# Kernel tuning notes

Measured on AMD Instinct MI355X. Metric: run time of the kernel, lower is better.

The kernel has to match this reference:

```python
import jax, jax.numpy as jnp
import numpy as np

NS = 100000   # served nodes
NI = 100000   # interfered nodes
E = 1000000   # edges per relation
D = 64        # 2 * Nt_num, Nt_num = 32
HM = 32       # message MLP hidden
HU = 16       # update MLP hidden


def _lin_init(key, fan_in, fan_out):
    s = 1.0 / np.sqrt(fan_in)
    kw, kb = jax.random.split(key)
    w = jax.random.uniform(kw, (fan_in, fan_out), jnp.float32, -s, s)
    b = jax.random.uniform(kb, (fan_out,), jnp.float32, -s, s)
    return w, b


def setup_inputs() -> dict:
    key = jax.random.key(0)
    ks = jax.random.split(key, 12)
    wm1, bm1 = _lin_init(ks[0], D, HM)
    wm2, bm2 = _lin_init(ks[1], HM, D)
    wu1, bu1 = _lin_init(ks[2], D, HU)
    wu2, bu2 = _lin_init(ks[3], HU, D)
    wo, bo = _lin_init(ks[4], D, D)
    edge_s2i = jnp.stack([
        jax.random.randint(ks[5], (E,), 0, NS),   # src in served
        jax.random.randint(ks[6], (E,), 0, NI),   # dst in interfered
    ]).astype(jnp.int64)
    edge_i2s = jnp.stack([
        jax.random.randint(ks[7], (E,), 0, NI),   # src in interfered
        jax.random.randint(ks[8], (E,), 0, NS),   # dst in served
    ]).astype(jnp.int64)
    return {
        "x_served": jax.random.normal(ks[9], (NS, D), jnp.float32),
        "x_interfered": jax.random.normal(ks[10], (NI, D), jnp.float32),
        "edge_s2i": edge_s2i,
        "edge_i2s": edge_i2s,
        "wm1": wm1, "bm1": bm1, "wm2": wm2, "bm2": bm2,
        "wu1": wu1, "bu1": bu1, "wu2": wu2, "bu2": bu2,
        "wo": wo, "bo": bo,
    }


def reference(x_served, x_interfered, edge_s2i, edge_i2s,
              wm1, bm1, wm2, bm2, wu1, bu1, wu2, bu2, wo, bo):
    def mlp_m(h):  # MLP([D, 32, D]): Lin+ReLU, Lin+ReLU
        return jax.nn.relu(jax.nn.relu(h @ wm1 + bm1) @ wm2 + bm2)

    def mlp_u(h):  # MLP([D, 16, D])
        return jax.nn.relu(jax.nn.relu(h @ wu1 + bu1) @ wu2 + bu2)

    def conv(x_src, edges, n_dst):
        # gather source node features per edge, per-edge message MLP
        msg = mlp_m(x_src[edges[0]])                    # [E, D]
        # scatter-sum into destination nodes
        agg = jax.ops.segment_sum(msg, edges[1], num_segments=n_dst)
        return mlp_u(agg)                               # [n_dst, D]

    xs, xi = x_served, x_interfered
    for _ in range(3):
        new_i = conv(xs, edge_s2i, NI)   # served -> interfered
        new_s = conv(xi, edge_i2s, NS)   # interfered -> served
        xs, xi = new_s, new_i
    # h2o on served: Lin + Tanh -> beamforming matrix
    return jnp.tanh(xs @ wo + bo)
```

## Files before the change

kernel.cpp:

```cpp
#include <hip/hip_runtime.h>
#include <hip/hip_fp16.h>
#include <math.h>

constexpr int D = 64;
constexpr int CAP = 48;
constexpr int RPB = 256;
constexpr int EPB = 8192;

typedef _Float16 half2_t __attribute__((ext_vector_type(2)));
typedef _Float16 f16x8 __attribute__((ext_vector_type(8)));
typedef float f32x4 __attribute__((ext_vector_type(4)));

__device__ inline float fdot2(unsigned a, unsigned b, float c){
    return __builtin_amdgcn_fdot2(__builtin_bit_cast(half2_t, a),
                                  __builtin_bit_cast(half2_t, b), c, false);
}

__device__ inline unsigned pack2(float lo, float hi){
    __half2 h = __floats2half2_rn(lo, hi);
    return *(unsigned*)&h;
}

__device__ inline void ld16u(const unsigned* base, unsigned* w){
    const uint4* p = (const uint4*)base;
    uint4 a = p[0], b = p[1], c = p[2], d = p[3];
    w[0]=a.x;  w[1]=a.y;  w[2]=a.z;  w[3]=a.w;
    w[4]=b.x;  w[5]=b.y;  w[6]=b.z;  w[7]=b.w;
    w[8]=c.x;  w[9]=c.y;  w[10]=c.z; w[11]=c.w;
    w[12]=d.x; w[13]=d.y; w[14]=d.z; w[15]=d.w;
}

__device__ inline void store_half8(__half* dst, const float* o){
    uint4 w;
    w.x = pack2(o[0], o[1]); w.y = pack2(o[2], o[3]);
    w.z = pack2(o[4], o[5]); w.w = pack2(o[6], o[7]);
    *((uint4*)dst) = w;
}

__device__ inline void load_half8(const __half* src, float* r){
    uint4 w = *((const uint4*)src);
    __half2* h = (__half2*)&w;
    float2 f0 = __half22float2(h[0]);
    float2 f1 = __half22float2(h[1]);
    float2 f2 = __half22float2(h[2]);
    float2 f3 = __half22float2(h[3]);
    r[0] = f0.x; r[1] = f0.y; r[2] = f1.x; r[3] = f1.y;
    r[4] = f2.x; r[5] = f2.y; r[6] = f3.x; r[7] = f3.y;
}


__global__ void k_zero(int* __restrict__ p, int n){
    for (int i = threadIdx.x; i < n; i += 256) p[i] = 0;
}


__global__ void __launch_bounds__(512) k_bucket_mlpm(
        const int* __restrict__ es2i, const int* __restrict__ ei2s, int E, int NI,
        int NBUK, int BSTRIDE,
        int* __restrict__ gcur, unsigned* __restrict__ buckets,
        const float* __restrict__ x,
        const float* __restrict__ wm1, const float* __restrict__ bm1,
        const float* __restrict__ wm2, const float* __restrict__ bm2,
        __half* __restrict__ y, int Nmlp, int nbEdge)
{
    __shared__ __align__(16) char smem[8704];
    int t = threadIdx.x;

    if ((int)blockIdx.x < nbEdge){
        int* hist = (int*)smem;
        int* base = (int*)(smem + 4096);
        for (int i = t; i < NBUK; i += 512) hist[i] = 0;
        __syncthreads();
        int e0 = blockIdx.x * EPB + t;
        int rr[16], ss[16];
        #pragma unroll
        for (int k = 0; k < 16; k++){
            int i = e0 + k*512;
            if (i < E){
                ss[k] = es2i[i];            rr[k] = es2i[E + i];
            } else if (i < 2*E){
                int j = i - E;
                ss[k] = ei2s[j];            rr[k] = NI + ei2s[E + j];
            } else rr[k] = -1;
        }
        #pragma unroll
        for (int k = 0; k < 16; k++)
            if (rr[k] >= 0) atomicAdd(&hist[rr[k] >> 8], 1);
        __syncthreads();
        for (int b = t; b < NBUK; b += 512){
            int h = hist[b];
            base[b] = h ? atomicAdd(&gcur[b], h) : 0;
        }
        __syncthreads();
        #pragma unroll
        for (int k = 0; k < 16; k++){
            if (rr[k] >= 0){
                int b = rr[k] >> 8;
                int p = atomicAdd(&base[b], 1);
                if (p < BSTRIDE)
                    buckets[(size_t)b*BSTRIDE + p] =
                        ((unsigned)(rr[k] & 255) << 24) | (unsigned)ss[k];
            }
        }
        return;
    }

    unsigned* w1p = (unsigned*)smem;
    unsigned* w2p = (unsigned*)(smem + 4096);
    float*    sb1 = (float*)(smem + 8192);
    float*    sb2 = (float*)(smem + 8320);
    for (int i = t; i < 1024; i += 512){ int kp=i>>5, j=i&31; w1p[i]=pack2(wm1[(2*kp)*32+j], wm1[(2*kp+1)*32+j]); }
    for (int i = t; i < 1024; i += 512){ int jp=i>>6, c=i&63; w2p[i]=pack2(wm2[(2*jp)*64+c], wm2[(2*jp+1)*64+c]); }
    if (t < 32) sb1[t] = bm1[t];
    else if (t >= 64 && t < 128) sb2[t - 64] = bm2[t - 64];
    __syncthreads();
    int n = ((int)blockIdx.x - nbEdge)*512 + t;
    if (n >= Nmlp) return;

    const float4* xp = (const float4*)(x + (size_t)n*D);
    unsigned xq[32];
    #pragma unroll
    for (int i = 0; i < 16; i++){
        float4 v = xp[i];
        xq[2*i]   = pack2(v.x, v.y);
        xq[2*i+1] = pack2(v.z, v.w);
    }
    float h[32];
    #pragma unroll
    for (int j = 0; j < 32; j++) h[j] = 0.f;
    #pragma unroll
    for (int kp = 0; kp < 32; kp++){
        unsigned xv = xq[kp];
        unsigned w[32];
        ld16u(&w1p[kp*32],      w);
        ld16u(&w1p[kp*32 + 16], w + 16);
        #pragma unroll
        for (int j = 0; j < 32; j++) h[j] = fdot2(xv, w[j], h[j]);
    }
    #pragma unroll
    for (int j = 0; j < 32; j++) h[j] = fmaxf(h[j] + sb1[j], 0.f);
    unsigned hh[16];
    #pragma unroll
    for (int jp = 0; jp < 16; jp++) hh[jp] = pack2(h[2*jp], h[2*jp+1]);

    __half* yrow = y + (size_t)n*D;
    #pragma unroll
    for (int c0 = 0; c0 < 64; c0 += 32){
        float o[32];
        #pragma unroll
        for (int c = 0; c < 32; c++) o[c] = sb2[c0 + c];
        #pragma unroll
        for (int jp = 0; jp < 16; jp++){
            unsigned hv = hh[jp];
            unsigned w[32];
            ld16u(&w2p[jp*64 + c0],      w);
            ld16u(&w2p[jp*64 + c0 + 16], w + 16);
            #pragma unroll
            for (int c = 0; c < 32; c++) o[c] = fdot2(hv, w[c], o[c]);
        }
        #pragma unroll
        for (int c = 0; c < 32; c++) o[c] = fmaxf(o[c], 0.f);
        store_half8(yrow + c0,      &o[0]);
        store_half8(yrow + c0 + 8,  &o[8]);
        store_half8(yrow + c0 + 16, &o[16]);
        store_half8(yrow + c0 + 24, &o[24]);
    }
}


__global__ void __launch_bounds__(512) k_scatter_lds(const int* __restrict__ gcur,
        const unsigned* __restrict__ buckets, int BSTRIDE, int NTOT,
        int* __restrict__ cnt, int* __restrict__ slots)
{
    __shared__ int lcnt[RPB];
    __shared__ int lslots[RPB*CAP];
    int t = threadIdx.x;
    int b = blockIdx.x;
    int r0 = b * RPB;
    int nrows = NTOT - r0; if (nrows > RPB) nrows = RPB;

    for (int i = t; i < RPB; i += 512) lcnt[i] = 0;
    __syncthreads();

    int n = gcur[b]; if (n > BSTRIDE) n = BSTRIDE;
    const unsigned* bp = buckets + (size_t)b*BSTRIDE;
    for (int k = t; k < n; k += 512){
        unsigned e = bp[k];
        int lr  = e >> 24;
        int src = e & 0xFFFFFF;
        int pos = atomicAdd(&lcnt[lr], 1);
        if (pos < CAP) lslots[lr*CAP + pos] = src;
    }
    __syncthreads();

    int4* gs = (int4*)(slots + (size_t)r0*CAP);
    const int4* ls = (const int4*)lslots;
    int n4 = nrows*CAP/4;
    for (int i = t; i < n4; i += 512) gs[i] = ls[i];
    for (int i = t; i < nrows; i += 512) cnt[r0 + i] = lcnt[i];
}


__global__ void __launch_bounds__(256) k_agg(const __half* __restrict__ M,
        const int* __restrict__ cnt, const int* __restrict__ slots,
        __half* __restrict__ agg, int N)
{
    int gid  = blockIdx.x*256 + threadIdx.x;
    int node = gid >> 6;
    if (node >= N) return;
    int lane = gid & 63;
    int sub  = lane >> 3;
    int fl   = lane & 7;
    int deg = cnt[node]; deg = deg < CAP ? deg : CAP;
    const int* row = slots + (size_t)node*CAP;
    float acc[8];
    #pragma unroll
    for (int i = 0; i < 8; i++) acc[i] = 0.f;
    for (int k = sub; k < deg; k += 8){
        int s = row[k];
        float v[8];
        load_half8(M + (size_t)s*D + fl*8, v);
        #pragma unroll
        for (int i = 0; i < 8; i++) acc[i] += v[i];
    }
    #pragma unroll
    for (int i = 0; i < 8; i++){
        acc[i] += __shfl_xor(acc[i], 8);
        acc[i] += __shfl_xor(acc[i], 16);
        acc[i] += __shfl_xor(acc[i], 32);
    }
    if (sub == 0) store_half8(agg + (size_t)node*D + fl*8, acc);
}


__global__ void __launch_bounds__(256) k_mlp_um(const __half* __restrict__ agg,
        const float* __restrict__ wu1, const float* __restrict__ bu1,
        const float* __restrict__ wu2, const float* __restrict__ bu2,
        const float* __restrict__ wm1, const float* __restrict__ bm1,
        const float* __restrict__ wm2, const float* __restrict__ bm2,
        __half* __restrict__ y, int N)
{
    __shared__ float  lds_h [4][16][20];
    __shared__ float  lds_y [4][16][68];
    __shared__ float  lds_hm[4][16][36];
    __shared__ __half lds_m [4][16][72];

    int t  = threadIdx.x;
    int wv = t >> 6, l = t & 63;
    int m  = l & 15, g = l >> 4;

    f16x8 Bu1[2], Bu2[4], Bm1[2][2], Bm2[4];
    #pragma unroll
    for (int kt = 0; kt < 2; kt++)
        #pragma unroll
        for (int i = 0; i < 8; i++)
            Bu1[kt][i] = (_Float16)wu1[(kt*32 + 8*g + i)*16 + m];
    #pragma unroll
    for (int jb = 0; jb < 4; jb++)
        #pragma unroll
        for (int i = 0; i < 8; i++){
            int k = 8*g + i;
            Bu2[jb][i] = (k < 16) ? (_Float16)wu2[k*64 + jb*16 + m] : (_Float16)0.f;
        }
    #pragma unroll
    for (int kt = 0; kt < 2; kt++)
        #pragma unroll
        for (int nt = 0; nt < 2; nt++)
            #pragma unroll
            for (int i = 0; i < 8; i++)
                Bm1[kt][nt][i] = (_Float16)wm1[(kt*32 + 8*g + i)*32 + nt*16 + m];
    #pragma unroll
    for (int jb = 0; jb < 4; jb++)
        #pragma unroll
        for (int i = 0; i < 8; i++)
            Bm2[jb][i] = (_Float16)wm2[(8*g + i)*64 + jb*16 + m];

    float bu1v = bu1[m];
    float bu2v[4], bm2v[4], bm1v[2];
    #pragma unroll
    for (int jb = 0; jb < 4; jb++){ bu2v[jb] = bu2[jb*16 + m]; bm2v[jb] = bm2[jb*16 + m]; }
    #pragma unroll
    for (int nt = 0; nt < 2; nt++) bm1v[nt] = bm1[nt*16 + m];

    #pragma unroll
    for (int tile = 0; tile < 2; tile++){
        int nb = blockIdx.x*128 + tile*64 + wv*16;
        if (nb >= N) break;

        int an = nb + m; if (an >= N) an = N - 1;
        const __half* arow = agg + (size_t)an*64;
        f16x8 Ax0 = *reinterpret_cast<const f16x8*>(arow + 8*g);
        f16x8 Ax1 = *reinterpret_cast<const f16x8*>(arow + 32 + 8*g);

        f32x4 acc = {0.f, 0.f, 0.f, 0.f};
        acc = __builtin_amdgcn_mfma_f32_16x16x32_f16(Ax0, Bu1[0], acc, 0, 0, 0);
        acc = __builtin_amdgcn_mfma_f32_16x16x32_f16(Ax1, Bu1[1], acc, 0, 0, 0);
        #pragma unroll
        for (int r = 0; r < 4; r++)
            lds_h[wv][4*g + r][m] = fmaxf(acc[r] + bu1v, 0.f);

        f16x8 Ah;
        #pragma unroll
        for (int i = 0; i < 8; i++){
            int k = 8*g + i;
            Ah[i] = (k < 16) ? (_Float16)lds_h[wv][m][k] : (_Float16)0.f;
        }

        #pragma unroll
        for (int jb = 0; jb < 4; jb++){
            f32x4 a2 = {0.f, 0.f, 0.f, 0.f};
            a2 = __builtin_amdgcn_mfma_f32_16x16x32_f16(Ah, Bu2[jb], a2, 0, 0, 0);
            #pragma unroll
            for (int r = 0; r < 4; r++)
                lds_y[wv][4*g + r][jb*16 + m] = fmaxf(a2[r] + bu2v[jb], 0.f);
        }

        f16x8 Ay0, Ay1;
        #pragma unroll
        for (int i = 0; i < 8; i++){
            Ay0[i] = (_Float16)lds_y[wv][m][8*g + i];
            Ay1[i] = (_Float16)lds_y[wv][m][32 + 8*g + i];
        }

        #pragma unroll
        for (int nt = 0; nt < 2; nt++){
            f32x4 a3 = {0.f, 0.f, 0.f, 0.f};
            a3 = __builtin_amdgcn_mfma_f32_16x16x32_f16(Ay0, Bm1[0][nt], a3, 0, 0, 0);
            a3 = __builtin_amdgcn_mfma_f32_16x16x32_f16(Ay1, Bm1[1][nt], a3, 0, 0, 0);
            #pragma unroll
            for (int r = 0; r < 4; r++)
                lds_hm[wv][4*g + r][nt*16 + m] = fmaxf(a3[r] + bm1v[nt], 0.f);
        }

        f16x8 Ahm;
        #pragma unroll
        for (int i = 0; i < 8; i++)
            Ahm[i] = (_Float16)lds_hm[wv][m][8*g + i];

        #pragma unroll
        for (int jb = 0; jb < 4; jb++){
            f32x4 a4 = {0.f, 0.f, 0.f, 0.f};
            a4 = __builtin_amdgcn_mfma_f32_16x16x32_f16(Ahm, Bm2[jb], a4, 0, 0, 0);
            #pragma unroll
            for (int r = 0; r < 4; r++)
                lds_m[wv][4*g + r][jb*16 + m] = __float2half(fmaxf(a4[r] + bm2v[jb], 0.f));
        }

        int lr = l >> 2;
        int node = nb + lr;
        if (node < N){
            uint4* dst = (uint4*)(y + (size_t)node*64);
            const uint4* src = (const uint4*)&lds_m[wv][lr][0];
            int c = l & 3;
            dst[c]     = src[c];
            dst[c + 4] = src[c + 4];
        }
    }
}


__device__ inline float fast_tanh(float x){
    float ax = fabsf(x);
    float e  = __expf(2.f*ax);
    float t  = 1.f - 2.f/(e + 1.f);
    return copysignf(t, x);
}

__global__ void __launch_bounds__(256) k_mlp_uo(const __half* __restrict__ agg,
        const float* __restrict__ wu1, const float* __restrict__ bu1,
        const float* __restrict__ wu2, const float* __restrict__ bu2,
        const float* __restrict__ wo,  const float* __restrict__ bo,
        float* __restrict__ out, int N)
{
    __shared__ float lds_h[4][16][20];
    __shared__ float lds_y[4][16][68];
    __shared__ float lds_o[4][16][68];

    int t  = threadIdx.x;
    int wv = t >> 6, l = t & 63;
    int m  = l & 15, g = l >> 4;

    f16x8 Bu1[2], Bu2[4], Bo[2][4];
    #pragma unroll
    for (int kt = 0; kt < 2; kt++)
        #pragma unroll
        for (int i = 0; i < 8; i++)
            Bu1[kt][i] = (_Float16)wu1[(kt*32 + 8*g + i)*16 + m];
    #pragma unroll
    for (int jb = 0; jb < 4; jb++)
        #pragma unroll
        for (int i = 0; i < 8; i++){
            int k = 8*g + i;
            Bu2[jb][i] = (k < 16) ? (_Float16)wu2[k*64 + jb*16 + m] : (_Float16)0.f;
        }
    #pragma unroll
    for (int kt = 0; kt < 2; kt++)
        #pragma unroll
        for (int jb = 0; jb < 4; jb++)
            #pragma unroll
            for (int i = 0; i < 8; i++)
                Bo[kt][jb][i] = (_Float16)wo[(kt*32 + 8*g + i)*64 + jb*16 + m];

    float bu1v = bu1[m];
    float bu2v[4], bov[4];
    #pragma unroll
    for (int jb = 0; jb < 4; jb++){ bu2v[jb] = bu2[jb*16 + m]; bov[jb] = bo[jb*16 + m]; }

    #pragma unroll
    for (int tile = 0; tile < 2; tile++){
        int nb = blockIdx.x*128 + tile*64 + wv*16;
        if (nb >= N) break;

        int an = nb + m; if (an >= N) an = N - 1;
        const __half* arow = agg + (size_t)an*64;
        f16x8 Ax0 = *reinterpret_cast<const f16x8*>(arow + 8*g);
        f16x8 Ax1 = *reinterpret_cast<const f16x8*>(arow + 32 + 8*g);

        f32x4 acc = {0.f, 0.f, 0.f, 0.f};
        acc = __builtin_amdgcn_mfma_f32_16x16x32_f16(Ax0, Bu1[0], acc, 0, 0, 0);
        acc = __builtin_amdgcn_mfma_f32_16x16x32_f16(Ax1, Bu1[1], acc, 0, 0, 0);
        #pragma unroll
        for (int r = 0; r < 4; r++)
            lds_h[wv][4*g + r][m] = fmaxf(acc[r] + bu1v, 0.f);

        f16x8 Ah;
        #pragma unroll
        for (int i = 0; i < 8; i++){
            int k = 8*g + i;
            Ah[i] = (k < 16) ? (_Float16)lds_h[wv][m][k] : (_Float16)0.f;
        }

        #pragma unroll
        for (int jb = 0; jb < 4; jb++){
            f32x4 a2 = {0.f, 0.f, 0.f, 0.f};
            a2 = __builtin_amdgcn_mfma_f32_16x16x32_f16(Ah, Bu2[jb], a2, 0, 0, 0);
            #pragma unroll
            for (int r = 0; r < 4; r++)
                lds_y[wv][4*g + r][jb*16 + m] = fmaxf(a2[r] + bu2v[jb], 0.f);
        }

        f16x8 Ay0, Ay1;
        #pragma unroll
        for (int i = 0; i < 8; i++){
            Ay0[i] = (_Float16)lds_y[wv][m][8*g + i];
            Ay1[i] = (_Float16)lds_y[wv][m][32 + 8*g + i];
        }

        #pragma unroll
        for (int jb = 0; jb < 4; jb++){
            f32x4 a3 = {0.f, 0.f, 0.f, 0.f};
            a3 = __builtin_amdgcn_mfma_f32_16x16x32_f16(Ay0, Bo[0][jb], a3, 0, 0, 0);
            a3 = __builtin_amdgcn_mfma_f32_16x16x32_f16(Ay1, Bo[1][jb], a3, 0, 0, 0);
            #pragma unroll
            for (int r = 0; r < 4; r++)
                lds_o[wv][4*g + r][jb*16 + m] = fast_tanh(a3[r] + bov[jb]);
        }

        int lr = l >> 2;
        int node = nb + lr;
        if (node < N){
            float4* dst = (float4*)(out + (size_t)node*64);
            const float4* src = (const float4*)&lds_o[wv][lr][0];
            int c = l & 3;
            dst[c]      = src[c];
            dst[c + 4]  = src[c + 4];
            dst[c + 8]  = src[c + 8];
            dst[c + 12] = src[c + 12];
        }
    }
}


extern "C" void kernel_launch(void* const* d_in, const int* in_sizes, int n_in,
                              void* d_out, int out_size, void* d_ws, size_t ws_size,
                              hipStream_t stream)
{
    const float* x_interfered = (const float*)d_in[1];
    const int*   e_s2i        = (const int*)d_in[2];
    const int*   e_i2s        = (const int*)d_in[3];
    const float* wm1 = (const float*)d_in[4];  const float* bm1 = (const float*)d_in[5];
    const float* wm2 = (const float*)d_in[6];  const float* bm2 = (const float*)d_in[7];
    const float* wu1 = (const float*)d_in[8];  const float* bu1 = (const float*)d_in[9];
    const float* wu2 = (const float*)d_in[10]; const float* bu2 = (const float*)d_in[11];
    const float* wo  = (const float*)d_in[12]; const float* bo  = (const float*)d_in[13];

    const int NS = in_sizes[0] / D;
    const int NI = in_sizes[1] / D;
    const int E  = in_sizes[2] / 2;
    const int NMAX = (NS > NI) ? NS : NI;
    const int NTOT = NI + NS;

    const int NBUK = ((NTOT - 1) >> 8) + 1;
    int avg = (2*E) / NBUK;
    const int BSTRIDE = ((2*avg) + 1023) & ~1023;

    char* p = (char*)d_ws;
    auto alloc = [&](size_t bytes) -> void* {
        void* r = (void*)p;
        p += (bytes + 255) & ~(size_t)255;
        return r;
    };
    __half*   M      = (__half*)alloc((size_t)NMAX*D*2);
    __half*   AGG    = (__half*)alloc((size_t)NMAX*D*2);
    int*      cnt    = (int*)alloc((size_t)NTOT*4);
    int*      gcur   = (int*)alloc((size_t)NBUK*4);
    int*      slots  = (int*)alloc((size_t)NTOT*CAP*4);
    unsigned* buckets= (unsigned*)alloc((size_t)NBUK*BSTRIDE*4);
    (void)ws_size; (void)n_in; (void)out_size;

    const int* cnt_i = cnt;
    const int* cnt_s = cnt + NI;
    const int* slots_i = slots;
    const int* slots_s = slots + (size_t)NI*CAP;

    k_zero<<<1, 256, 0, stream>>>(gcur, NBUK);

    const int nbEdge = (2*E + EPB - 1)/EPB;
    const int nbMlp  = (NI + 511)/512;
    k_bucket_mlpm<<<nbEdge + nbMlp, 512, 0, stream>>>(
        e_s2i, e_i2s, E, NI, NBUK, BSTRIDE, gcur, buckets,
        x_interfered, wm1, bm1, wm2, bm2, M, NI, nbEdge);
    k_scatter_lds<<<NBUK, 512, 0, stream>>>(gcur, buckets, BSTRIDE, NTOT, cnt, slots);

    k_agg<<<((size_t)NS*64 + 255)/256, 256, 0, stream>>>(M, cnt_s, slots_s, AGG, NS);
    k_mlp_um<<<(NS + 127)/128, 256, 0, stream>>>(AGG, wu1, bu1, wu2, bu2,
                                               wm1, bm1, wm2, bm2, M, NS);
    k_agg<<<((size_t)NI*64 + 255)/256, 256, 0, stream>>>(M, cnt_i, slots_i, AGG, NI);
    k_mlp_um<<<(NI + 127)/128, 256, 0, stream>>>(AGG, wu1, bu1, wu2, bu2,
                                               wm1, bm1, wm2, bm2, M, NI);
    k_agg<<<((size_t)NS*64 + 255)/256, 256, 0, stream>>>(M, cnt_s, slots_s, AGG, NS);
    k_mlp_uo<<<(NS + 127)/128, 256, 0, stream>>>(AGG, wu1, bu1, wu2, bu2,
                                               wo, bo, (float*)d_out, NS);
}
```

Before: 219.7 us.

## Fuse neighbor aggregation into update/message MLP kernels with ping-pong buffers

Removes the separate aggregation kernel and performs the gather-sum of neighbor messages inside the MLP kernel, writing the aggregate to LDS instead of global memory. Each lane group now sums a 16-feature slice serially over all neighbors of one node, and double buffers replace the in-place M/AGG pair. This drops an intermediate global round-trip and three launches. In exchange, aggregation parallelism per node falls: 4 lanes per node walk the degree loop sequentially instead of 64 lanes splitting edges, which lengthens the gather latency chain.

```diff
diff --git a/kernel.cpp b/kernel.cpp
--- a/kernel.cpp
+++ b/kernel.cpp
@@ -10,11 +10,6 @@
 typedef _Float16 half2_t __attribute__((ext_vector_type(2)));
 typedef _Float16 f16x8 __attribute__((ext_vector_type(8)));
 typedef float f32x4 __attribute__((ext_vector_type(4)));
-
-__device__ inline float fdot2(unsigned a, unsigned b, float c){
-    return __builtin_amdgcn_fdot2(__builtin_bit_cast(half2_t, a),
-                                  __builtin_bit_cast(half2_t, b), c, false);
-}
 
 __device__ inline unsigned pack2(float lo, float hi){
     __half2 h = __floats2half2_rn(lo, hi);
@@ -28,6 +23,11 @@
     w[4]=b.x;  w[5]=b.y;  w[6]=b.z;  w[7]=b.w;
     w[8]=c.x;  w[9]=c.y;  w[10]=c.z; w[11]=c.w;
     w[12]=d.x; w[13]=d.y; w[14]=d.z; w[15]=d.w;
+}
+
+__device__ inline float fdot2(unsigned a, unsigned b, float c){
+    return __builtin_amdgcn_fdot2(__builtin_bit_cast(half2_t, a),
+                                  __builtin_bit_cast(half2_t, b), c, false);
 }
 
 __device__ inline void store_half8(__half* dst, const float* o){
@@ -201,45 +201,15 @@
 }
 
 
-__global__ void __launch_bounds__(256) k_agg(const __half* __restrict__ M,
+__global__ void __launch_bounds__(256) k_conv_um(const __half* __restrict__ Msrc,
         const int* __restrict__ cnt, const int* __restrict__ slots,
-        __half* __restrict__ agg, int N)
-{
-    int gid  = blockIdx.x*256 + threadIdx.x;
-    int node = gid >> 6;
-    if (node >= N) return;
-    int lane = gid & 63;
-    int sub  = lane >> 3;
-    int fl   = lane & 7;
-    int deg = cnt[node]; deg = deg < CAP ? deg : CAP;
-    const int* row = slots + (size_t)node*CAP;
-    float acc[8];
-    #pragma unroll
-    for (int i = 0; i < 8; i++) acc[i] = 0.f;
-    for (int k = sub; k < deg; k += 8){
-        int s = row[k];
-        float v[8];
-        load_half8(M + (size_t)s*D + fl*8, v);
-        #pragma unroll
-        for (int i = 0; i < 8; i++) acc[i] += v[i];
-    }
-    #pragma unroll
-    for (int i = 0; i < 8; i++){
-        acc[i] += __shfl_xor(acc[i], 8);
-        acc[i] += __shfl_xor(acc[i], 16);
-        acc[i] += __shfl_xor(acc[i], 32);
-    }
-    if (sub == 0) store_half8(agg + (size_t)node*D + fl*8, acc);
-}
-
-
-__global__ void __launch_bounds__(256) k_mlp_um(const __half* __restrict__ agg,
         const float* __restrict__ wu1, const float* __restrict__ bu1,
         const float* __restrict__ wu2, const float* __restrict__ bu2,
         const float* __restrict__ wm1, const float* __restrict__ bm1,
         const float* __restrict__ wm2, const float* __restrict__ bm2,
-        __half* __restrict__ y, int N)
+        __half* __restrict__ Mdst, int N)
 {
+    __shared__ __half lds_x [4][16][72];
     __shared__ float  lds_h [4][16][20];
     __shared__ float  lds_y [4][16][68];
     __shared__ float  lds_hm[4][16][36];
@@ -287,17 +257,35 @@
         int nb = blockIdx.x*128 + tile*64 + wv*16;
         if (nb >= N) break;
 
-        int an = nb + m; if (an >= N) an = N - 1;
-        const __half* arow = agg + (size_t)an*64;
-        f16x8 Ax0 = *reinterpret_cast<const f16x8*>(arow + 8*g);
-        f16x8 Ax1 = *reinterpret_cast<const f16x8*>(arow + 32 + 8*g);
-
-        f32x4 acc = {0.f, 0.f, 0.f, 0.f};
-        acc = __builtin_amdgcn_mfma_f32_16x16x32_f16(Ax0, Bu1[0], acc, 0, 0, 0);
-        acc = __builtin_amdgcn_mfma_f32_16x16x32_f16(Ax1, Bu1[1], acc, 0, 0, 0);
+        float acc[16];
+        #pragma unroll
+        for (int i = 0; i < 16; i++) acc[i] = 0.f;
+        int node = nb + m;
+        if (node < N){
+            int deg = cnt[node]; deg = deg < CAP ? deg : CAP;
+            const int* row = slots + (size_t)node*CAP;
+            for (int k = 0; k < deg; k++){
+                int s = row[k];
+                const __half* mr = Msrc + (size_t)s*64 + g*16;
+                float v[16];
+                load_half8(mr,     v);
+                load_half8(mr + 8, v + 8);
+                #pragma unroll
+                for (int i = 0; i < 16; i++) acc[i] += v[i];
+            }
+        }
+        store_half8(&lds_x[wv][m][g*16],     acc);
+        store_half8(&lds_x[wv][m][g*16 + 8], acc + 8);
+
+        f16x8 Ax0 = *reinterpret_cast<const f16x8*>(&lds_x[wv][m][8*g]);
+        f16x8 Ax1 = *reinterpret_cast<const f16x8*>(&lds_x[wv][m][32 + 8*g]);
+
+        f32x4 a1 = {0.f, 0.f, 0.f, 0.f};
+        a1 = __builtin_amdgcn_mfma_f32_16x16x32_f16(Ax0, Bu1[0], a1, 0, 0, 0);
+        a1 = __builtin_amdgcn_mfma_f32_16x16x32_f16(Ax1, Bu1[1], a1, 0, 0, 0);
         #pragma unroll
         for (int r = 0; r < 4; r++)
-            lds_h[wv][4*g + r][m] = fmaxf(acc[r] + bu1v, 0.f);
+            lds_h[wv][4*g + r][m] = fmaxf(a1[r] + bu1v, 0.f);
 
         f16x8 Ah;
         #pragma unroll
@@ -347,9 +335,9 @@
         }
 
         int lr = l >> 2;
-        int node = nb + lr;
-        if (node < N){
-            uint4* dst = (uint4*)(y + (size_t)node*64);
+        int wnode = nb + lr;
+        if (wnode < N){
+            uint4* dst = (uint4*)(Mdst + (size_t)wnode*64);
             const uint4* src = (const uint4*)&lds_m[wv][lr][0];
             int c = l & 3;
             dst[c]     = src[c];
@@ -366,15 +354,17 @@
     return copysignf(t, x);
 }
 
-__global__ void __launch_bounds__(256) k_mlp_uo(const __half* __restrict__ agg,
+__global__ void __launch_bounds__(256) k_conv_uo(const __half* __restrict__ Msrc,
+        const int* __restrict__ cnt, const int* __restrict__ slots,
         const float* __restrict__ wu1, const float* __restrict__ bu1,
         const float* __restrict__ wu2, const float* __restrict__ bu2,
         const float* __restrict__ wo,  const float* __restrict__ bo,
         float* __restrict__ out, int N)
 {
-    __shared__ float lds_h[4][16][20];
-    __shared__ float lds_y[4][16][68];
-    __shared__ float lds_o[4][16][68];
+    __shared__ __half lds_x[4][16][72];
+    __shared__ float  lds_h[4][16][20];
+    __shared__ float  lds_y[4][16][68];
+    __shared__ float  lds_o[4][16][68];
 
     int t  = threadIdx.x;
     int wv = t >> 6, l = t & 63;
@@ -411,17 +401,35 @@
         int nb = blockIdx.x*128 + tile*64 + wv*16;
         if (nb >= N) break;
 
-        int an = nb + m; if (an >= N) an = N - 1;
-        const __half* arow = agg + (size_t)an*64;
-        f16x8 Ax0 = *reinterpret_cast<const f16x8*>(arow + 8*g);
-        f16x8 Ax1 = *reinterpret_cast<const f16x8*>(arow + 32 + 8*g);
-
-        f32x4 acc = {0.f, 0.f, 0.f, 0.f};
-        acc = __builtin_amdgcn_mfma_f32_16x16x32_f16(Ax0, Bu1[0], acc, 0, 0, 0);
-        acc = __builtin_amdgcn_mfma_f32_16x16x32_f16(Ax1, Bu1[1], acc, 0, 0, 0);
+        float acc[16];
+        #pragma unroll
+        for (int i = 0; i < 16; i++) acc[i] = 0.f;
+        int node = nb + m;
+        if (node < N){
+            int deg = cnt[node]; deg = deg < CAP ? deg : CAP;
+            const int* row = slots + (size_t)node*CAP;
+            for (int k = 0; k < deg; k++){
+                int s = row[k];
+                const __half* mr = Msrc + (size_t)s*64 + g*16;
+                float v[16];
+                load_half8(mr,     v);
+                load_half8(mr + 8, v + 8);
+                #pragma unroll
+                for (int i = 0; i < 16; i++) acc[i] += v[i];
+            }
+        }
+        store_half8(&lds_x[wv][m][g*16],     acc);
+        store_half8(&lds_x[wv][m][g*16 + 8], acc + 8);
+
+        f16x8 Ax0 = *reinterpret_cast<const f16x8*>(&lds_x[wv][m][8*g]);
+        f16x8 Ax1 = *reinterpret_cast<const f16x8*>(&lds_x[wv][m][32 + 8*g]);
+
+        f32x4 a1 = {0.f, 0.f, 0.f, 0.f};
+        a1 = __builtin_amdgcn_mfma_f32_16x16x32_f16(Ax0, Bu1[0], a1, 0, 0, 0);
+        a1 = __builtin_amdgcn_mfma_f32_16x16x32_f16(Ax1, Bu1[1], a1, 0, 0, 0);
         #pragma unroll
         for (int r = 0; r < 4; r++)
-            lds_h[wv][4*g + r][m] = fmaxf(acc[r] + bu1v, 0.f);
+            lds_h[wv][4*g + r][m] = fmaxf(a1[r] + bu1v, 0.f);
 
         f16x8 Ah;
         #pragma unroll
@@ -457,9 +465,9 @@
         }
 
         int lr = l >> 2;
-        int node = nb + lr;
-        if (node < N){
-            float4* dst = (float4*)(out + (size_t)node*64);
+        int wnode = nb + lr;
+        if (wnode < N){
+            float4* dst = (float4*)(out + (size_t)wnode*64);
             const float4* src = (const float4*)&lds_o[wv][lr][0];
             int c = l & 3;
             dst[c]      = src[c];
@@ -500,8 +508,8 @@
         p += (bytes + 255) & ~(size_t)255;
         return r;
     };
-    __half*   M      = (__half*)alloc((size_t)NMAX*D*2);
-    __half*   AGG    = (__half*)alloc((size_t)NMAX*D*2);
+    __half*   MA     = (__half*)alloc((size_t)NMAX*D*2);
+    __half*   MB     = (__half*)alloc((size_t)NMAX*D*2);
     int*      cnt    = (int*)alloc((size_t)NTOT*4);
     int*      gcur   = (int*)alloc((size_t)NBUK*4);
     int*      slots  = (int*)alloc((size_t)NTOT*CAP*4);
@@ -519,16 +527,13 @@
     const int nbMlp  = (NI + 511)/512;
     k_bucket_mlpm<<<nbEdge + nbMlp, 512, 0, stream>>>(
         e_s2i, e_i2s, E, NI, NBUK, BSTRIDE, gcur, buckets,
-        x_interfered, wm1, bm1, wm2, bm2, M, NI, nbEdge);
+        x_interfered, wm1, bm1, wm2, bm2, MA, NI, nbEdge);
     k_scatter_lds<<<NBUK, 512, 0, stream>>>(gcur, buckets, BSTRIDE, NTOT, cnt, slots);
 
-    k_agg<<<((size_t)NS*64 + 255)/256, 256, 0, stream>>>(M, cnt_s, slots_s, AGG, NS);
-    k_mlp_um<<<(NS + 127)/128, 256, 0, stream>>>(AGG, wu1, bu1, wu2, bu2,
-                                               wm1, bm1, wm2, bm2, M, NS);
-    k_agg<<<((size_t)NI*64 + 255)/256, 256, 0, stream>>>(M, cnt_i, slots_i, AGG, NI);
-    k_mlp_um<<<(NI + 127)/128, 256, 0, stream>>>(AGG, wu1, bu1, wu2, bu2,
-                                               wm1, bm1, wm2, bm2, M, NI);
-    k_agg<<<((size_t)NS*64 + 255)/256, 256, 0, stream>>>(M, cnt_s, slots_s, AGG, NS);
-    k_mlp_uo<<<(NS + 127)/128, 256, 0, stream>>>(AGG, wu1, bu1, wu2, bu2,
-                                               wo, bo, (float*)d_out, NS);
-}
+    k_conv_um<<<(NS + 127)/128, 256, 0, stream>>>(MA, cnt_s, slots_s,
+        wu1, bu1, wu2, bu2, wm1, bm1, wm2, bm2, MB, NS);
+    k_conv_um<<<(NI + 127)/128, 256, 0, stream>>>(MB, cnt_i, slots_i,
+        wu1, bu1, wu2, bu2, wm1, bm1, wm2, bm2, MA, NI);
+    k_conv_uo<<<(NS + 127)/128, 256, 0, stream>>>(MA, cnt_s, slots_s,
+        wu1, bu1, wu2, bu2, wo, bo, (float*)d_out, NS);
+}
```

New measurement: 263.8 us. +20.0%, slower.
